# Performance work log

Measured on AMD Instinct MI355X. Metric: run time of the kernel, lower is better.

## Reference

```python
import jax, jax.numpy as jnp
import numpy as np

N_NODES = 50000
N_EDGES = 800000
D = 128          # node/edge feature dim
H = 128          # MLP hidden dim
T_EDGE = 3       # number of edge types
T_NODE = 2       # number of node types


def setup_inputs() -> dict:
    key = jax.random.key(0)
    ks = jax.random.split(key, 14)
    s = 0.05  # weight init scale
    return {
        "nf": jax.random.normal(ks[0], (N_NODES, D), jnp.float32),
        "ef": jax.random.normal(ks[1], (N_EDGES, D), jnp.float32),
        "src": jax.random.randint(ks[2], (N_EDGES,), 0, N_NODES, jnp.int32),
        "dst": jax.random.randint(ks[3], (N_EDGES,), 0, N_NODES, jnp.int32),
        "etype": jax.random.randint(ks[4], (N_EDGES,), 0, T_EDGE, jnp.int32),
        "ntype": jax.random.randint(ks[5], (N_NODES,), 0, T_NODE, jnp.int32),
        # per-edge-type MLP: Linear(3D->H), ReLU, Linear(H->D)
        "We_h": jax.random.normal(ks[6], (T_EDGE, 3 * D, H), jnp.float32) * s,
        "be_h": jnp.zeros((T_EDGE, H), jnp.float32),
        "We_o": jax.random.normal(ks[7], (T_EDGE, H, D), jnp.float32) * s,
        "be_o": jnp.zeros((T_EDGE, D), jnp.float32),
        # per-node-type MLP: Linear(2D->H), ReLU, Linear(H->D)
        "Wn_h": jax.random.normal(ks[8], (T_NODE, 2 * D, H), jnp.float32) * s,
        "bn_h": jnp.zeros((T_NODE, H), jnp.float32),
        "Wn_o": jax.random.normal(ks[9], (T_NODE, H, D), jnp.float32) * s,
        "bn_o": jnp.zeros((T_NODE, D), jnp.float32),
    }


def _typed_mlp(x, tvec, Wh, bh, Wo, bo):
    """Per-type 2-layer MLP dispatch, then the source's gather-back.

    The torch code builds type_pos_list (stable concat of per-type index lists,
    i.e. a stable argsort of tvec) and then indexes the concatenated per-type
    outputs with that same permutation (`updated[type_perm]`, a gather rather
    than an inverse-permutation scatter). We reproduce that exactly:
    out_final[j] = out_correct[perm[perm[j]]].
    """
    T = Wh.shape[0]
    out = jnp.zeros((x.shape[0], Wo.shape[-1]), x.dtype)
    for k in range(T):  # small fixed number of types
        y = jax.nn.relu(x @ Wh[k] + bh[k]) @ Wo[k] + bo[k]
        out = jnp.where((tvec == k)[:, None], y, out)
    perm = jnp.argsort(tvec)  # jax argsort is stable
    return out[perm[perm]]


def reference(nf, ef, src, dst, etype, ntype,
              We_h, be_h, We_o, be_o, Wn_h, bn_h, Wn_o, bn_o):
    # edge update: cat([ef, src_nf, dst_nf]) -> per-type MLP
    em_in = jnp.concatenate([ef, nf[src], nf[dst]], axis=-1)  # [E, 3D]
    new_ef = _typed_mlp(em_in, etype, We_h, be_h, We_o, be_o)  # [E, D]
    # message passing: copy_e('h') messages, sum reduce into dst nodes
    agg_m = jax.ops.segment_sum(new_ef, dst, num_segments=nf.shape[0])  # [N, D]
    # node update: cat([agg_m, nf]) -> per-type MLP
    nm_in = jnp.concatenate([agg_m, nf], axis=-1)  # [N, 2D]
    new_nf = _typed_mlp(nm_in, ntype, Wn_h, bn_h, Wn_o, bn_o)  # [N, D]
    return new_nf, new_ef
```

## Files before the change

kernel.cpp:

```cpp
#include <hip/hip_runtime.h>

typedef __bf16 bf16_t;
typedef bf16_t bf16x8_t __attribute__((ext_vector_type(8)));
typedef float  f32x4_t  __attribute__((ext_vector_type(4)));

#define RCHUNK 4096

__global__ void pack_w_kernel(const float* __restrict__ W, bf16_t* __restrict__ out,
                              int T, int Ksrc, int k0, int KB)
{
  int total = T * KB * 8 * 512;
  for (int idx = blockIdx.x * blockDim.x + threadIdx.x; idx < total;
       idx += gridDim.x * blockDim.x) {
    int j  = idx & 7;
    int l  = (idx >> 3) & 63;
    int nb = (idx >> 9) & 7;
    int r  = idx >> 12;
    int kb = r % KB;
    int t  = r / KB;
    int k = k0 + kb * 32 + ((l >> 4) << 3) + j;
    int n = nb * 16 + (l & 15);
    out[idx] = (bf16_t)W[((size_t)t * Ksrc + k) * 128 + n];
  }
}

template <int T>
__global__ void count_types_kernel(const int* __restrict__ tv, int n,
                                   int* __restrict__ blkcnt)
{
  __shared__ int cnt[T];
  int tid = threadIdx.x, b = blockIdx.x;
  if (tid < T) cnt[tid] = 0;
  __syncthreads();
  int lo = b * RCHUNK, hi = min(n, lo + RCHUNK);
  int loc[T];
#pragma unroll
  for (int t = 0; t < T; ++t) loc[t] = 0;
  for (int i = lo + tid; i < hi; i += 256) {
    int tq = tv[i];
#pragma unroll
    for (int t = 0; t < T; ++t) loc[t] += (tq == t);
  }
#pragma unroll
  for (int t = 0; t < T; ++t)
    if (loc[t]) atomicAdd(&cnt[t], loc[t]);
  __syncthreads();
  if (tid < T) blkcnt[b * T + tid] = cnt[tid];
}

template <int T>
__global__ void scan_blocks_kernel(const int* __restrict__ blkcnt, int nblocks,
                                   int* __restrict__ blkbase)
{
  __shared__ int sh[256];
  __shared__ int tot[T];
  int tid = threadIdx.x;
  int myc[T], excl[T];
#pragma unroll
  for (int t = 0; t < T; ++t) myc[t] = (tid < nblocks) ? blkcnt[tid * T + t] : 0;
#pragma unroll
  for (int t = 0; t < T; ++t) {
    sh[tid] = myc[t];
    __syncthreads();
    for (int off = 1; off < 256; off <<= 1) {
      int v = (tid >= off) ? sh[tid - off] : 0;
      __syncthreads();
      sh[tid] += v;
      __syncthreads();
    }
    excl[t] = sh[tid] - myc[t];
    if (tid == 255) tot[t] = sh[255];
    __syncthreads();
  }
  if (tid < nblocks) {
    int run = 0;
#pragma unroll
    for (int t = 0; t < T; ++t) {
      blkbase[tid * T + t] = run + excl[t];
      run += tot[t];
    }
  }
}

template <int T>
__global__ void write_ranks_kernel(const int* __restrict__ tv, int n,
                                   const int* __restrict__ blkbase,
                                   int* __restrict__ rank, int* __restrict__ perm)
{
  __shared__ int sh[256];
  int tid = threadIdx.x, b = blockIdx.x;
  int lo = b * RCHUNK + tid * 16;
  int tvq[16];
  int myc[T];
#pragma unroll
  for (int t = 0; t < T; ++t) myc[t] = 0;
#pragma unroll
  for (int q = 0; q < 16; ++q) {
    int i = lo + q;
    int tq = (i < n) ? tv[i] : -1;
    tvq[q] = tq;
#pragma unroll
    for (int t = 0; t < T; ++t) myc[t] += (tq == t);
  }
  int mybase[T];
#pragma unroll
  for (int t = 0; t < T; ++t) {
    sh[tid] = myc[t];
    __syncthreads();
    for (int off = 1; off < 256; off <<= 1) {
      int v = (tid >= off) ? sh[tid - off] : 0;
      __syncthreads();
      sh[tid] += v;
      __syncthreads();
    }
    mybase[t] = blkbase[b * T + t] + sh[tid] - myc[t];
    __syncthreads();
  }
#pragma unroll
  for (int q = 0; q < 16; ++q) {
    int tq = tvq[q];
    if (tq < 0) continue;
    int r = 0;
#pragma unroll
    for (int t = 0; t < T; ++t)
      if (tq == t) { r = mybase[t]; mybase[t] = r + 1; }
    rank[lo + q] = r;
    perm[r] = lo + q;
  }
}

__global__ void hist_dst_kernel(const int* __restrict__ dst, int E,
                                int* __restrict__ hist)
{
  int i = blockIdx.x * blockDim.x + threadIdx.x;
  if (i < E) atomicAdd(&hist[dst[i]], 1);
}

__global__ __launch_bounds__(1024) void scan_offsets_kernel(
    const int* __restrict__ hist, int n, int* __restrict__ offsets,
    int* __restrict__ cursor)
{
  __shared__ int sh[1024];
  int tid = threadIdx.x;
  int per = (n + 1023) >> 10;
  int lo = tid * per;
  int s = 0;
  for (int q = 0; q < per; ++q) {
    int i = lo + q;
    if (i < n) s += hist[i];
  }
  sh[tid] = s;
  __syncthreads();
  for (int off = 1; off < 1024; off <<= 1) {
    int v = (tid >= off) ? sh[tid - off] : 0;
    __syncthreads();
    sh[tid] += v;
    __syncthreads();
  }
  int run = sh[tid] - s;
  for (int q = 0; q < per; ++q) {
    int i = lo + q;
    if (i < n) {
      offsets[i] = run;
      cursor[i] = run;
      run += hist[i];
    }
  }
  if (tid == 1023) offsets[n] = sh[1023];
}

__global__ void scatter_dst_kernel(const int* __restrict__ dst, int E,
                                   int* __restrict__ cursor,
                                   int* __restrict__ edge_by_dst)
{
  int i = blockIdx.x * blockDim.x + threadIdx.x;
  if (i < E) {
    int pos = atomicAdd(&cursor[dst[i]], 1);
    edge_by_dst[pos] = i;
  }
}

__global__ __launch_bounds__(256) void aggregate_kernel(
    const float* __restrict__ ef_new, const int* __restrict__ edge_by_dst,
    const int* __restrict__ offsets, float* __restrict__ agg, int Nn)
{
  int gwid = (blockIdx.x * 256 + threadIdx.x) >> 6;
  int l = threadIdx.x & 63;
  int nw = (gridDim.x * 256) >> 6;
  for (int n = gwid; n < Nn; n += nw) {
    int lo = offsets[n], hi = offsets[n + 1];
    float sx = 0.f, sy = 0.f;
    int q = lo;
    for (; q + 1 < hi; q += 2) {
      int e0 = edge_by_dst[q], e1 = edge_by_dst[q + 1];
      float2 v0 = *(const float2*)(ef_new + (size_t)e0 * 128 + l * 2);
      float2 v1 = *(const float2*)(ef_new + (size_t)e1 * 128 + l * 2);
      sx += v0.x + v1.x;
      sy += v0.y + v1.y;
    }
    if (q < hi) {
      int e0 = edge_by_dst[q];
      float2 v0 = *(const float2*)(ef_new + (size_t)e0 * 128 + l * 2);
      sx += v0.x;
      sy += v0.y;
    }
    float2 o;
    o.x = sx; o.y = sy;
    *(float2*)(agg + (size_t)n * 128 + l * 2) = o;
  }
}

__global__ __launch_bounds__(256) void precompute_p_kernel(
    const float* __restrict__ nf,
    const bf16_t* __restrict__ pW1s, const bf16_t* __restrict__ pW1d,
    const bf16_t* __restrict__ pWn1b,
    bf16_t* __restrict__ Ps, bf16_t* __restrict__ Pd, bf16_t* __restrict__ Pn,
    int Nn)
{
  __shared__ char Wsm[32768];
  const int which = blockIdx.x & 7, tile = blockIdx.x >> 3;
  const bf16_t* pB; bf16_t* po;
  if (which < 3)      { pB = pW1s + which * 16384;        po = Ps + (size_t)which * Nn * 128; }
  else if (which < 6) { pB = pW1d + (which - 3) * 16384;  po = Pd + (size_t)(which - 3) * Nn * 128; }
  else                { pB = pWn1b + (which - 6) * 16384; po = Pn + (size_t)(which - 6) * Nn * 128; }

  const int tid = threadIdx.x, l = tid & 63, w = tid >> 6;
  const int rb = (w >> 1) * 32, cb = (w & 1) * 64, l15 = l & 15;
  const int koff = (l >> 4) << 3;

  {
    const uint4* g = (const uint4*)pB;
    uint4* d = (uint4*)Wsm;
#pragma unroll
    for (int q = 0; q < 8; ++q) d[q * 256 + tid] = g[q * 256 + tid];
  }

  const int base = tile * 64;
  const int r0 = base + rb + l15, r1 = r0 + 16;
  const float* q0 = nf + (size_t)min(r0, Nn - 1) * 128 + koff;
  const float* q1 = nf + (size_t)min(r1, Nn - 1) * 128 + koff;
  f32x4_t areg[2][4][2];
#pragma unroll
  for (int kb = 0; kb < 4; ++kb) {
    areg[0][kb][0] = ((const f32x4_t*)(q0 + kb * 32))[0];
    areg[0][kb][1] = ((const f32x4_t*)(q0 + kb * 32))[1];
    areg[1][kb][0] = ((const f32x4_t*)(q1 + kb * 32))[0];
    areg[1][kb][1] = ((const f32x4_t*)(q1 + kb * 32))[1];
  }
  __syncthreads();

  f32x4_t acc[2][4];
#pragma unroll
  for (int m = 0; m < 2; ++m)
#pragma unroll
    for (int n = 0; n < 4; ++n) acc[m][n] = (f32x4_t){0.f, 0.f, 0.f, 0.f};

#pragma unroll
  for (int kb = 0; kb < 4; ++kb) {
    bf16x8_t bfr[4];
#pragma unroll
    for (int n = 0; n < 4; ++n)
      bfr[n] = *(const bf16x8_t*)(Wsm + ((kb * 8 + (cb >> 4) + n) * 64 + l) * 16);
    bf16x8_t a0, a1;
#pragma unroll
    for (int z = 0; z < 4; ++z) {
      a0[z] = (bf16_t)areg[0][kb][0][z]; a0[4 + z] = (bf16_t)areg[0][kb][1][z];
      a1[z] = (bf16_t)areg[1][kb][0][z]; a1[4 + z] = (bf16_t)areg[1][kb][1][z];
    }
#pragma unroll
    for (int n = 0; n < 4; ++n) {
      acc[0][n] = __builtin_amdgcn_mfma_f32_16x16x32_bf16(a0, bfr[n], acc[0][n], 0, 0, 0);
      acc[1][n] = __builtin_amdgcn_mfma_f32_16x16x32_bf16(a1, bfr[n], acc[1][n], 0, 0, 0);
    }
  }

#pragma unroll
  for (int n = 0; n < 4; ++n) {
    int col = cb + 16 * n + l15;
#pragma unroll
    for (int m = 0; m < 2; ++m)
#pragma unroll
      for (int jj = 0; jj < 4; ++jj) {
        int row = rb + 16 * m + ((l >> 4) << 2) + jj;
        int node = base + row;
        if (node < Nn) po[(size_t)node * 128 + col] = (bf16_t)acc[m][n][jj];
      }
  }
}

template <int T, bool EDGE>
__global__ __launch_bounds__(256, 2) void mlp4_kernel(
    const float* __restrict__ feat,
    const int* __restrict__ src, const int* __restrict__ dst,
    const int* __restrict__ perm, const int* __restrict__ rank,
    const int* __restrict__ tbase,
    const bf16_t* __restrict__ pW1, const float* __restrict__ b1,
    const bf16_t* __restrict__ pW2, const float* __restrict__ b2,
    const bf16_t* __restrict__ P1, const bf16_t* __restrict__ P2, int pnodes,
    float* __restrict__ out, int Ntot)
{
  __shared__ char Wsm[32768];
  __shared__ char Psm[16384];
  __shared__ char Hsm[16384];
  __shared__ int sm_e[64], sm_j[64], sm_s0[64], sm_s1[64];

  const int tid = threadIdx.x;
  const int l = tid & 63, w = tid >> 6;
  const int rb = (w >> 1) * 32, cb = (w & 1) * 64;
  const int l15 = l & 15;
  const int koff = (l >> 4) << 3;

  const int s0 = tbase[0];
  const int s1 = (T > 1) ? tbase[1] : Ntot;
  const int s2 = (T > 2) ? tbase[2] : Ntot;
  const int e0t = (T > 1) ? s1 : Ntot;
  const int e1t = (T > 2) ? s2 : Ntot;
  const int c0 = (e0t - s0 + 63) >> 6;
  const int c1 = (T > 1) ? ((e1t - s1 + 63) >> 6) : 0;
  const int c2 = (T > 2) ? ((Ntot - s2 + 63) >> 6) : 0;
  const int cum1 = c0, cum2 = c0 + c1, total = cum2 + c2;

  const int tpb = (total + gridDim.x - 1) / gridDim.x;
  const int pt0 = blockIdx.x * tpb;
  const int pt1 = min(total, pt0 + tpb);

  int cur_t = -1;
  bf16x8_t w2r[16];
  float bh[4], bo[4];

  for (int pt = pt0; pt < pt1; ++pt) {
    const int t = (pt < cum1) ? 0 : ((pt < cum2) ? 1 : 2);
    const int tstart = (t == 0) ? s0 : ((t == 1) ? s1 : s2);
    const int tend = (t == 0) ? e0t : ((t == 1) ? e1t : Ntot);
    const int i = pt - ((t == 0) ? 0 : ((t == 1) ? cum1 : cum2));
    const int pbase = tstart + (i << 6);

    __syncthreads();
    if (tid < 64) {
      int pos = pbase + tid;
      if (pos < tend) {
        int e = perm[pos];
        sm_e[tid] = e;
        sm_j[tid] = rank[pos];
        if (EDGE) { sm_s0[tid] = src[e]; sm_s1[tid] = dst[e]; }
      } else {
        sm_e[tid] = 0; sm_j[tid] = -1;
        if (EDGE) { sm_s0[tid] = 0; sm_s1[tid] = 0; }
      }
    }
    __syncthreads();

    const int ar0 = rb + l15, ar1 = ar0 + 16;
    const float* q0 = feat + (size_t)sm_e[ar0] * 128 + koff;
    const float* q1 = feat + (size_t)sm_e[ar1] * 128 + koff;
    f32x4_t areg[2][4][2];
#pragma unroll
    for (int kb = 0; kb < 4; ++kb) {
      areg[0][kb][0] = ((const f32x4_t*)(q0 + kb * 32))[0];
      areg[0][kb][1] = ((const f32x4_t*)(q0 + kb * 32))[1];
      areg[1][kb][0] = ((const f32x4_t*)(q1 + kb * 32))[0];
      areg[1][kb][1] = ((const f32x4_t*)(q1 + kb * 32))[1];
    }

#pragma unroll
    for (int q = 0; q < 4; ++q) {
      int idx = tid * 4 + q;
      int row = idx >> 4, c8 = idx & 15;
      bf16x8_t s;
      if (EDGE) {
        bf16x8_t u = ((const bf16x8_t*)(P1 + ((size_t)t * pnodes + sm_s0[row]) * 128))[c8];
        bf16x8_t v = ((const bf16x8_t*)(P2 + ((size_t)t * pnodes + sm_s1[row]) * 128))[c8];
#pragma unroll
        for (int z = 0; z < 8; ++z) s[z] = (bf16_t)((float)u[z] + (float)v[z]);
      } else {
        s = ((const bf16x8_t*)(P1 + ((size_t)t * pnodes + sm_e[row]) * 128))[c8];
      }
      *(bf16x8_t*)(Psm + row * 256 + ((c8 ^ (row & 15)) << 4)) = s;
    }

    if (t != cur_t) {
      __syncthreads();
      {
        const uint4* g = (const uint4*)(pW1 + (size_t)t * 16384);
        uint4* d = (uint4*)Wsm;
#pragma unroll
        for (int q = 0; q < 8; ++q) d[q * 256 + tid] = g[q * 256 + tid];
      }
      {
        const bf16x8_t* g2 = (const bf16x8_t*)pW2;
#pragma unroll
        for (int kb = 0; kb < 4; ++kb)
#pragma unroll
          for (int n = 0; n < 4; ++n)
            w2r[kb * 4 + n] = g2[(size_t)((t * 4 + kb) * 8 + (cb >> 4) + n) * 64 + l];
      }
#pragma unroll
      for (int n = 0; n < 4; ++n) {
        bh[n] = b1[t * 128 + cb + 16 * n + l15];
        bo[n] = b2[t * 128 + cb + 16 * n + l15];
      }
      cur_t = t;
      __syncthreads();
    }

    f32x4_t acc[2][4];
#pragma unroll
    for (int m = 0; m < 2; ++m)
#pragma unroll
      for (int n = 0; n < 4; ++n) acc[m][n] = (f32x4_t){0.f, 0.f, 0.f, 0.f};

#pragma unroll
    for (int kb = 0; kb < 4; ++kb) {
      bf16x8_t bfr[4];
#pragma unroll
      for (int n = 0; n < 4; ++n)
        bfr[n] = *(const bf16x8_t*)(Wsm + ((kb * 8 + (cb >> 4) + n) * 64 + l) * 16);
      bf16x8_t a0, a1;
#pragma unroll
      for (int z = 0; z < 4; ++z) {
        a0[z] = (bf16_t)areg[0][kb][0][z]; a0[4 + z] = (bf16_t)areg[0][kb][1][z];
        a1[z] = (bf16_t)areg[1][kb][0][z]; a1[4 + z] = (bf16_t)areg[1][kb][1][z];
      }
#pragma unroll
      for (int n = 0; n < 4; ++n) {
        acc[0][n] = __builtin_amdgcn_mfma_f32_16x16x32_bf16(a0, bfr[n], acc[0][n], 0, 0, 0);
        acc[1][n] = __builtin_amdgcn_mfma_f32_16x16x32_bf16(a1, bfr[n], acc[1][n], 0, 0, 0);
      }
    }

    __syncthreads();
#pragma unroll
    for (int n = 0; n < 4; ++n) {
      int col = cb + 16 * n + l15;
      int byte = col * 2;
#pragma unroll
      for (int m = 0; m < 2; ++m)
#pragma unroll
        for (int jj = 0; jj < 4; ++jj) {
          int row = rb + 16 * m + ((l >> 4) << 2) + jj;
          float pv = (float)*(const bf16_t*)(
              Psm + row * 256 + ((byte & 15) | ((((byte >> 4) ^ (row & 15)) & 15) << 4)));
          float v = acc[m][n][jj] + pv + bh[n];
          v = v > 0.f ? v : 0.f;
          *(bf16_t*)(Hsm + row * 256 + (byte ^ ((row & 7) << 4))) = (bf16_t)v;
        }
    }
    __syncthreads();

    f32x4_t acc2[2][4];
#pragma unroll
    for (int m = 0; m < 2; ++m)
#pragma unroll
      for (int n = 0; n < 4; ++n) acc2[m][n] = (f32x4_t){0.f, 0.f, 0.f, 0.f};

#pragma unroll
    for (int kb = 0; kb < 4; ++kb) {
      int kbyte = kb * 64 + ((l >> 4) << 4);
      int row0 = rb + l15, row1 = row0 + 16;
      bf16x8_t h0 = *(const bf16x8_t*)(Hsm + row0 * 256 + (kbyte ^ ((row0 & 7) << 4)));
      bf16x8_t h1 = *(const bf16x8_t*)(Hsm + row1 * 256 + (kbyte ^ ((row1 & 7) << 4)));
#pragma unroll
      for (int n = 0; n < 4; ++n) {
        acc2[0][n] = __builtin_amdgcn_mfma_f32_16x16x32_bf16(h0, w2r[kb * 4 + n], acc2[0][n], 0, 0, 0);
        acc2[1][n] = __builtin_amdgcn_mfma_f32_16x16x32_bf16(h1, w2r[kb * 4 + n], acc2[1][n], 0, 0, 0);
      }
    }

#pragma unroll
    for (int n = 0; n < 4; ++n) {
      int col = cb + 16 * n + l15;
#pragma unroll
      for (int m = 0; m < 2; ++m)
#pragma unroll
        for (int jj = 0; jj < 4; ++jj) {
          int row = rb + 16 * m + ((l >> 4) << 2) + jj;
          int j = sm_j[row];
          if (j >= 0) out[(size_t)j * 128 + col] = acc2[m][n][jj] + bo[n];
        }
    }
  }
}

extern "C" void kernel_launch(void* const* d_in, const int* in_sizes, int n_in,
                              void* d_out, int out_size, void* d_ws, size_t ws_size,
                              hipStream_t stream)
{
  const float* nf    = (const float*)d_in[0];
  const float* ef    = (const float*)d_in[1];
  const int*   src   = (const int*)d_in[2];
  const int*   dst   = (const int*)d_in[3];
  const int*   etype = (const int*)d_in[4];
  const int*   ntype = (const int*)d_in[5];
  const float* Weh   = (const float*)d_in[6];
  const float* beh   = (const float*)d_in[7];
  const float* Weo   = (const float*)d_in[8];
  const float* beo   = (const float*)d_in[9];
  const float* Wnh   = (const float*)d_in[10];
  const float* bnh   = (const float*)d_in[11];
  const float* Wno   = (const float*)d_in[12];
  const float* bno   = (const float*)d_in[13];

  const int E = in_sizes[2];
  const int N = in_sizes[5];
  const int TE = 3, TN = 2;

  char* ws = (char*)d_ws;
  size_t off = 0;
  auto alloc = [&](size_t bytes) -> char* {
    char* p = ws + off;
    off = (off + bytes + 511) & ~(size_t)511;
    return p;
  };
  bf16_t* pW1e  = (bf16_t*)alloc((size_t)TE * 16384 * 2);
  bf16_t* pW1s  = (bf16_t*)alloc((size_t)TE * 16384 * 2);
  bf16_t* pW1d  = (bf16_t*)alloc((size_t)TE * 16384 * 2);
  bf16_t* pWe2  = (bf16_t*)alloc((size_t)TE * 16384 * 2);
  bf16_t* pWn1a = (bf16_t*)alloc((size_t)TN * 16384 * 2);
  bf16_t* pWn1b = (bf16_t*)alloc((size_t)TN * 16384 * 2);
  bf16_t* pWn2  = (bf16_t*)alloc((size_t)TN * 16384 * 2);
  bf16_t* Ps = (bf16_t*)alloc((size_t)TE * N * 128 * 2);
  bf16_t* Pd = (bf16_t*)alloc((size_t)TE * N * 128 * 2);
  bf16_t* Pn = (bf16_t*)alloc((size_t)TN * N * 128 * 2);
  int* rank_e = (int*)alloc((size_t)E * 4);
  int* perm_e = (int*)alloc((size_t)E * 4);
  int* rank_n = (int*)alloc((size_t)N * 4);
  int* perm_n = (int*)alloc((size_t)N * 4);
  const int NBE = (E + RCHUNK - 1) / RCHUNK;
  const int NBN = (N + RCHUNK - 1) / RCHUNK;
  int* blkcnt_e  = (int*)alloc((size_t)NBE * TE * 4);
  int* blkbase_e = (int*)alloc((size_t)NBE * TE * 4);
  int* blkcnt_n  = (int*)alloc((size_t)NBN * TN * 4);
  int* blkbase_n = (int*)alloc((size_t)NBN * TN * 4);
  float* agg = (float*)alloc((size_t)N * 128 * 4);
  int* dsthist     = (int*)alloc((size_t)N * 4);
  int* dstoffs     = (int*)alloc((size_t)(N + 1) * 4);
  int* dstcursor   = (int*)alloc((size_t)N * 4);
  int* edge_by_dst = (int*)alloc((size_t)E * 4);
  (void)ws_size; (void)n_in; (void)out_size;

  pack_w_kernel<<<192, 256, 0, stream>>>(Weh, pW1e, TE, 384, 0, 4);
  pack_w_kernel<<<192, 256, 0, stream>>>(Weh, pW1s, TE, 384, 128, 4);
  pack_w_kernel<<<192, 256, 0, stream>>>(Weh, pW1d, TE, 384, 256, 4);
  pack_w_kernel<<<192, 256, 0, stream>>>(Weo, pWe2, TE, 128, 0, 4);
  pack_w_kernel<<<128, 256, 0, stream>>>(Wnh, pWn1a, TN, 256, 0, 4);
  pack_w_kernel<<<128, 256, 0, stream>>>(Wnh, pWn1b, TN, 256, 128, 4);
  pack_w_kernel<<<128, 256, 0, stream>>>(Wno, pWn2, TN, 128, 0, 4);

  const int ptiles = (N + 63) / 64;
  precompute_p_kernel<<<ptiles * 8, 256, 0, stream>>>(
      nf, pW1s, pW1d, pWn1b, Ps, Pd, Pn, N);

  count_types_kernel<3><<<NBE, 256, 0, stream>>>(etype, E, blkcnt_e);
  scan_blocks_kernel<3><<<1, 256, 0, stream>>>(blkcnt_e, NBE, blkbase_e);
  write_ranks_kernel<3><<<NBE, 256, 0, stream>>>(etype, E, blkbase_e, rank_e, perm_e);

  count_types_kernel<2><<<NBN, 256, 0, stream>>>(ntype, N, blkcnt_n);
  scan_blocks_kernel<2><<<1, 256, 0, stream>>>(blkcnt_n, NBN, blkbase_n);
  write_ranks_kernel<2><<<NBN, 256, 0, stream>>>(ntype, N, blkbase_n, rank_n, perm_n);

  hipMemsetAsync(dsthist, 0, (size_t)N * 4, stream);
  hist_dst_kernel<<<(E + 255) / 256, 256, 0, stream>>>(dst, E, dsthist);
  scan_offsets_kernel<<<1, 1024, 0, stream>>>(dsthist, N, dstoffs, dstcursor);
  scatter_dst_kernel<<<(E + 255) / 256, 256, 0, stream>>>(dst, E, dstcursor, edge_by_dst);

  float* out_nf = (float*)d_out;
  float* out_ef = (float*)d_out + (size_t)N * 128;

  mlp4_kernel<3, true><<<512, 256, 0, stream>>>(
      ef, src, dst, perm_e, rank_e, blkbase_e,
      pW1e, beh, pWe2, beo, Ps, Pd, N, out_ef, E);

  aggregate_kernel<<<3200, 256, 0, stream>>>(out_ef, edge_by_dst, dstoffs, agg, N);

  mlp4_kernel<2, false><<<512, 256, 0, stream>>>(
      agg, nullptr, nullptr, perm_n, rank_n, blkbase_n,
      pWn1a, bnh, pWn2, bno, Pn, nullptr, N, out_nf, N);
}
```

Before: 840.2 us.

## Sort edges by (type,dst) and aggregate from a contiguous bf16 slot buffer

Edges within each type segment are reordered by destination node through a key histogram, scan and scatter, and the per-edge metadata (edge id, src, dst, rank) is packed into one int4 array that the MLP kernel reads. The edge MLP also writes a bf16 copy of each output row into a slot buffer in processing order, so aggregation reads contiguous runs instead of gathering fp32 rows at random. This cuts the bytes and randomness of the aggregation reads, at the cost of extra bf16 writes, a larger key space for the scan, and bf16 rounding of the messages before summation.

```diff
diff --git a/kernel.cpp b/kernel.cpp
--- a/kernel.cpp
+++ b/kernel.cpp
@@ -1,10 +1,12 @@
 #include <hip/hip_runtime.h>
 
 typedef __bf16 bf16_t;
+typedef bf16_t bf16x2_t __attribute__((ext_vector_type(2)));
 typedef bf16_t bf16x8_t __attribute__((ext_vector_type(8)));
 typedef float  f32x4_t  __attribute__((ext_vector_type(4)));
 
 #define RCHUNK 4096
+#define MFMA16(a, b, c) __builtin_amdgcn_mfma_f32_16x16x32_bf16((a), (b), (c), 0, 0, 0)
 
 __global__ void pack_w_kernel(const float* __restrict__ W, bf16_t* __restrict__ out,
                               int T, int Ksrc, int k0, int KB)
@@ -129,11 +131,18 @@
   }
 }
 
-__global__ void hist_dst_kernel(const int* __restrict__ dst, int E,
-                                int* __restrict__ hist)
-{
-  int i = blockIdx.x * blockDim.x + threadIdx.x;
-  if (i < E) atomicAdd(&hist[dst[i]], 1);
+__global__ void key_hist_kernel(const int* __restrict__ rank,
+                                const int* __restrict__ dst,
+                                const int* __restrict__ tb, int E, int Nn,
+                                int* __restrict__ key, int* __restrict__ khist)
+{
+  int pos = blockIdx.x * blockDim.x + threadIdx.x;
+  if (pos < E) {
+    int t = (pos >= tb[1]) + (pos >= tb[2]);
+    int k = t * Nn + dst[rank[pos]];
+    key[pos] = k;
+    atomicAdd(&khist[k], 1);
+  }
 }
 
 __global__ __launch_bounds__(1024) void scan_offsets_kernel(
@@ -169,43 +178,64 @@
   if (tid == 1023) offsets[n] = sh[1023];
 }
 
-__global__ void scatter_dst_kernel(const int* __restrict__ dst, int E,
-                                   int* __restrict__ cursor,
-                                   int* __restrict__ edge_by_dst)
+__global__ void kscatter_meta_kernel(const int* __restrict__ key,
+                                     const int* __restrict__ perm,
+                                     const int* __restrict__ rank,
+                                     const int* __restrict__ src,
+                                     const int* __restrict__ dst,
+                                     int* __restrict__ kcursor,
+                                     int4* __restrict__ meta4, int E)
+{
+  int pos = blockIdx.x * blockDim.x + threadIdx.x;
+  if (pos < E) {
+    int slotp = atomicAdd(&kcursor[key[pos]], 1);
+    int e = perm[pos];
+    int4 m;
+    m.x = e; m.y = src[e]; m.z = dst[e]; m.w = rank[pos];
+    meta4[slotp] = m;
+  }
+}
+
+__global__ void gather_meta_node_kernel(const int* __restrict__ perm,
+                                        const int* __restrict__ rank,
+                                        int4* __restrict__ meta4, int N)
 {
   int i = blockIdx.x * blockDim.x + threadIdx.x;
-  if (i < E) {
-    int pos = atomicAdd(&cursor[dst[i]], 1);
-    edge_by_dst[pos] = i;
-  }
-}
-
-__global__ __launch_bounds__(256) void aggregate_kernel(
-    const float* __restrict__ ef_new, const int* __restrict__ edge_by_dst,
-    const int* __restrict__ offsets, float* __restrict__ agg, int Nn)
-{
-  int gwid = (blockIdx.x * 256 + threadIdx.x) >> 6;
+  if (i < N) {
+    int e = perm[i];
+    int4 m;
+    m.x = e; m.y = e; m.z = e; m.w = rank[i];
+    meta4[i] = m;
+  }
+}
+
+__global__ __launch_bounds__(256) void aggregate_runs_kernel(
+    const bf16_t* __restrict__ slot_buf, const int* __restrict__ koffs,
+    float* __restrict__ agg, int Nn)
+{
+  int gw = (blockIdx.x * 256 + threadIdx.x) >> 6;
   int l = threadIdx.x & 63;
   int nw = (gridDim.x * 256) >> 6;
-  for (int n = gwid; n < Nn; n += nw) {
-    int lo = offsets[n], hi = offsets[n + 1];
+  for (int n = gw; n < Nn; n += nw) {
     float sx = 0.f, sy = 0.f;
-    int q = lo;
-    for (; q + 1 < hi; q += 2) {
-      int e0 = edge_by_dst[q], e1 = edge_by_dst[q + 1];
-      float2 v0 = *(const float2*)(ef_new + (size_t)e0 * 128 + l * 2);
-      float2 v1 = *(const float2*)(ef_new + (size_t)e1 * 128 + l * 2);
-      sx += v0.x + v1.x;
-      sy += v0.y + v1.y;
-    }
-    if (q < hi) {
-      int e0 = edge_by_dst[q];
-      float2 v0 = *(const float2*)(ef_new + (size_t)e0 * 128 + l * 2);
-      sx += v0.x;
-      sy += v0.y;
-    }
-    float2 o;
-    o.x = sx; o.y = sy;
+#pragma unroll
+    for (int t = 0; t < 3; ++t) {
+      int k = t * Nn + n;
+      int lo = koffs[k], hi = koffs[k + 1];
+      int q = lo;
+      for (; q + 1 < hi; q += 2) {
+        bf16x2_t v0 = *(const bf16x2_t*)(slot_buf + (size_t)q * 128 + l * 2);
+        bf16x2_t v1 = *(const bf16x2_t*)(slot_buf + (size_t)(q + 1) * 128 + l * 2);
+        sx += (float)v0[0] + (float)v1[0];
+        sy += (float)v0[1] + (float)v1[1];
+      }
+      if (q < hi) {
+        bf16x2_t v0 = *(const bf16x2_t*)(slot_buf + (size_t)q * 128 + l * 2);
+        sx += (float)v0[0];
+        sy += (float)v0[1];
+      }
+    }
+    float2 o; o.x = sx; o.y = sy;
     *(float2*)(agg + (size_t)n * 128 + l * 2) = o;
   }
 }
@@ -236,16 +266,17 @@
   }
 
   const int base = tile * 64;
-  const int r0 = base + rb + l15, r1 = r0 + 16;
-  const float* q0 = nf + (size_t)min(r0, Nn - 1) * 128 + koff;
-  const float* q1 = nf + (size_t)min(r1, Nn - 1) * 128 + koff;
-  f32x4_t areg[2][4][2];
+  const int r0 = min(base + rb + l15, Nn - 1);
+  const int r1 = min(base + rb + l15 + 16, Nn - 1);
+  const float* q0 = nf + (size_t)r0 * 128 + koff;
+  const float* q1 = nf + (size_t)r1 * 128 + koff;
+  f32x4_t areg[16];
 #pragma unroll
   for (int kb = 0; kb < 4; ++kb) {
-    areg[0][kb][0] = ((const f32x4_t*)(q0 + kb * 32))[0];
-    areg[0][kb][1] = ((const f32x4_t*)(q0 + kb * 32))[1];
-    areg[1][kb][0] = ((const f32x4_t*)(q1 + kb * 32))[0];
-    areg[1][kb][1] = ((const f32x4_t*)(q1 + kb * 32))[1];
+    areg[kb * 2]     = ((const f32x4_t*)(q0 + kb * 32))[0];
+    areg[kb * 2 + 1] = ((const f32x4_t*)(q0 + kb * 32))[1];
+    areg[8 + kb * 2]     = ((const f32x4_t*)(q1 + kb * 32))[0];
+    areg[8 + kb * 2 + 1] = ((const f32x4_t*)(q1 + kb * 32))[1];
   }
   __syncthreads();
 
@@ -264,13 +295,13 @@
     bf16x8_t a0, a1;
 #pragma unroll
     for (int z = 0; z < 4; ++z) {
-      a0[z] = (bf16_t)areg[0][kb][0][z]; a0[4 + z] = (bf16_t)areg[0][kb][1][z];
-      a1[z] = (bf16_t)areg[1][kb][0][z]; a1[4 + z] = (bf16_t)areg[1][kb][1][z];
+      a0[z] = (bf16_t)areg[kb * 2][z];     a0[4 + z] = (bf16_t)areg[kb * 2 + 1][z];
+      a1[z] = (bf16_t)areg[8 + kb * 2][z]; a1[4 + z] = (bf16_t)areg[8 + kb * 2 + 1][z];
     }
 #pragma unroll
     for (int n = 0; n < 4; ++n) {
-      acc[0][n] = __builtin_amdgcn_mfma_f32_16x16x32_bf16(a0, bfr[n], acc[0][n], 0, 0, 0);
-      acc[1][n] = __builtin_amdgcn_mfma_f32_16x16x32_bf16(a1, bfr[n], acc[1][n], 0, 0, 0);
+      acc[0][n] = MFMA16(a0, bfr[n], acc[0][n]);
+      acc[1][n] = MFMA16(a1, bfr[n], acc[1][n]);
     }
   }
 
@@ -289,15 +320,14 @@
 }
 
 template <int T, bool EDGE>
-__global__ __launch_bounds__(256, 2) void mlp4_kernel(
+__global__ __launch_bounds__(256, 2) void mlp6_kernel(
     const float* __restrict__ feat,
-    const int* __restrict__ src, const int* __restrict__ dst,
-    const int* __restrict__ perm, const int* __restrict__ rank,
+    const int4* __restrict__ meta4,
     const int* __restrict__ tbase,
     const bf16_t* __restrict__ pW1, const float* __restrict__ b1,
     const bf16_t* __restrict__ pW2, const float* __restrict__ b2,
     const bf16_t* __restrict__ P1, const bf16_t* __restrict__ P2, int pnodes,
-    float* __restrict__ out, int Ntot)
+    float* __restrict__ out, bf16_t* __restrict__ slot_out, int Ntot)
 {
   __shared__ char Wsm[32768];
   __shared__ char Psm[16384];
@@ -339,10 +369,10 @@
     if (tid < 64) {
       int pos = pbase + tid;
       if (pos < tend) {
-        int e = perm[pos];
-        sm_e[tid] = e;
-        sm_j[tid] = rank[pos];
-        if (EDGE) { sm_s0[tid] = src[e]; sm_s1[tid] = dst[e]; }
+        int4 m = meta4[pos];
+        sm_e[tid] = m.x;
+        sm_j[tid] = m.w;
+        if (EDGE) { sm_s0[tid] = m.y; sm_s1[tid] = m.z; }
       } else {
         sm_e[tid] = 0; sm_j[tid] = -1;
         if (EDGE) { sm_s0[tid] = 0; sm_s1[tid] = 0; }
@@ -423,8 +453,8 @@
       }
 #pragma unroll
       for (int n = 0; n < 4; ++n) {
-        acc[0][n] = __builtin_amdgcn_mfma_f32_16x16x32_bf16(a0, bfr[n], acc[0][n], 0, 0, 0);
-        acc[1][n] = __builtin_amdgcn_mfma_f32_16x16x32_bf16(a1, bfr[n], acc[1][n], 0, 0, 0);
+        acc[0][n] = MFMA16(a0, bfr[n], acc[0][n]);
+        acc[1][n] = MFMA16(a1, bfr[n], acc[1][n]);
       }
     }
 
@@ -461,8 +491,8 @@
       bf16x8_t h1 = *(const bf16x8_t*)(Hsm + row1 * 256 + (kbyte ^ ((row1 & 7) << 4)));
 #pragma unroll
       for (int n = 0; n < 4; ++n) {
-        acc2[0][n] = __builtin_amdgcn_mfma_f32_16x16x32_bf16(h0, w2r[kb * 4 + n], acc2[0][n], 0, 0, 0);
-        acc2[1][n] = __builtin_amdgcn_mfma_f32_16x16x32_bf16(h1, w2r[kb * 4 + n], acc2[1][n], 0, 0, 0);
+        acc2[0][n] = MFMA16(h0, w2r[kb * 4 + n], acc2[0][n]);
+        acc2[1][n] = MFMA16(h1, w2r[kb * 4 + n], acc2[1][n]);
       }
     }
 
@@ -475,7 +505,12 @@
         for (int jj = 0; jj < 4; ++jj) {
           int row = rb + 16 * m + ((l >> 4) << 2) + jj;
           int j = sm_j[row];
-          if (j >= 0) out[(size_t)j * 128 + col] = acc2[m][n][jj] + bo[n];
+          if (j >= 0) {
+            float v = acc2[m][n][jj] + bo[n];
+            out[(size_t)j * 128 + col] = v;
+            if (EDGE)
+              slot_out[(size_t)(pbase + row) * 128 + col] = (bf16_t)v;
+          }
         }
     }
   }
@@ -532,10 +567,14 @@
   int* blkcnt_n  = (int*)alloc((size_t)NBN * TN * 4);
   int* blkbase_n = (int*)alloc((size_t)NBN * TN * 4);
   float* agg = (float*)alloc((size_t)N * 128 * 4);
-  int* dsthist     = (int*)alloc((size_t)N * 4);
-  int* dstoffs     = (int*)alloc((size_t)(N + 1) * 4);
-  int* dstcursor   = (int*)alloc((size_t)N * 4);
-  int* edge_by_dst = (int*)alloc((size_t)E * 4);
+  const int NK = TE * N;
+  int* key     = (int*)alloc((size_t)E * 4);
+  int* khist   = (int*)alloc((size_t)NK * 4);
+  int* koffs   = (int*)alloc((size_t)(NK + 1) * 4);
+  int* kcursor = (int*)alloc((size_t)NK * 4);
+  int4* meta4_e = (int4*)alloc((size_t)E * 16);
+  int4* meta4_n = (int4*)alloc((size_t)N * 16);
+  bf16_t* slot_buf = (bf16_t*)alloc((size_t)E * 128 * 2);
   (void)ws_size; (void)n_in; (void)out_size;
 
   pack_w_kernel<<<192, 256, 0, stream>>>(Weh, pW1e, TE, 384, 0, 4);
@@ -558,21 +597,26 @@
   scan_blocks_kernel<2><<<1, 256, 0, stream>>>(blkcnt_n, NBN, blkbase_n);
   write_ranks_kernel<2><<<NBN, 256, 0, stream>>>(ntype, N, blkbase_n, rank_n, perm_n);
 
-  hipMemsetAsync(dsthist, 0, (size_t)N * 4, stream);
-  hist_dst_kernel<<<(E + 255) / 256, 256, 0, stream>>>(dst, E, dsthist);
-  scan_offsets_kernel<<<1, 1024, 0, stream>>>(dsthist, N, dstoffs, dstcursor);
-  scatter_dst_kernel<<<(E + 255) / 256, 256, 0, stream>>>(dst, E, dstcursor, edge_by_dst);
+  hipMemsetAsync(khist, 0, (size_t)NK * 4, stream);
+  key_hist_kernel<<<(E + 255) / 256, 256, 0, stream>>>(
+      rank_e, dst, blkbase_e, E, N, key, khist);
+  scan_offsets_kernel<<<1, 1024, 0, stream>>>(khist, NK, koffs, kcursor);
+  kscatter_meta_kernel<<<(E + 255) / 256, 256, 0, stream>>>(
+      key, perm_e, rank_e, src, dst, kcursor, meta4_e, E);
+
+  gather_meta_node_kernel<<<(N + 255) / 256, 256, 0, stream>>>(
+      perm_n, rank_n, meta4_n, N);
 
   float* out_nf = (float*)d_out;
   float* out_ef = (float*)d_out + (size_t)N * 128;
 
-  mlp4_kernel<3, true><<<512, 256, 0, stream>>>(
-      ef, src, dst, perm_e, rank_e, blkbase_e,
-      pW1e, beh, pWe2, beo, Ps, Pd, N, out_ef, E);
-
-  aggregate_kernel<<<3200, 256, 0, stream>>>(out_ef, edge_by_dst, dstoffs, agg, N);
-
-  mlp4_kernel<2, false><<<512, 256, 0, stream>>>(
-      agg, nullptr, nullptr, perm_n, rank_n, blkbase_n,
-      pWn1a, bnh, pWn2, bno, Pn, nullptr, N, out_nf, N);
-}
+  mlp6_kernel<3, true><<<512, 256, 0, stream>>>(
+      ef, meta4_e, blkbase_e,
+      pW1e, beh, pWe2, beo, Ps, Pd, N, out_ef, slot_buf, E);
+
+  aggregate_runs_kernel<<<3200, 256, 0, stream>>>(slot_buf, koffs, agg, N);
+
+  mlp6_kernel<2, false><<<512, 256, 0, stream>>>(
+      agg, meta4_n, blkbase_n,
+      pWn1a, bnh, pWn2, bno, Pn, nullptr, N, out_nf, nullptr, N);
+}
```

Result: slower. 1.160 ms (+38.0%).
